# Optimization experiments

Hardware: AMD Instinct MI355X
Metric: run time of the kernel (lower is better)

## Reference

```python
import jax, jax.numpy as jnp
import numpy as np

TEMP = 0.07
W00 = 0.1
EPS = 1e-8


def setup_inputs() -> dict:
    key = jax.random.key(0)
    k1, k2, k3, k4 = jax.random.split(key, 4)
    B, N, D = 32, 256, 256
    M = B * N
    return {
        "audio_feats": jax.random.normal(k1, (B, N, D), dtype=jnp.float32),
        "visual_feats": jax.random.normal(k2, (B, N, D), dtype=jnp.float32),
        "audio_labels": jax.random.randint(k3, (M,), 0, 2, dtype=jnp.int64)
            if jax.config.jax_enable_x64 else jax.random.randint(k3, (M,), 0, 2, dtype=jnp.int32),
        "visual_labels": jax.random.randint(k4, (M,), 0, 2, dtype=jnp.int64)
            if jax.config.jax_enable_x64 else jax.random.randint(k4, (M,), 0, 2, dtype=jnp.int32),
    }


def reference(audio_feats, visual_feats, audio_labels, visual_labels):
    B, N, D = audio_feats.shape
    M = B * N
    a = audio_feats.reshape(M, D)
    v = visual_feats.reshape(M, D)
    # L2 normalize (torch F.normalize uses eps=1e-12 clamp on norm)
    a = a / jnp.maximum(jnp.linalg.norm(a, axis=-1, keepdims=True), 1e-12)
    v = v / jnp.maximum(jnp.linalg.norm(v, axis=-1, keepdims=True), 1e-12)
    sim = (a @ v.T) / TEMP  # (M, M)
    exp_sim = jnp.exp(sim)
    la = audio_labels[:, None]  # (M, 1)
    lv = visual_labels[None, :]  # (1, M)
    pos_mask = (la == lv) & ((la == 1) | (la == 0))
    weight = jnp.where(la == 1, 1.0, W00) * pos_mask.astype(sim.dtype)  # (M, M)
    wexp = exp_sim * weight

    # audio -> visual (row direction)
    denom_a2v = exp_sim.sum(axis=1)
    num_a2v = wexp.sum(axis=1)
    frac_a2v = (num_a2v + EPS) / (denom_a2v + EPS)
    valid_a2v = (num_a2v > 0).astype(sim.dtype)
    loss_a2v = -(valid_a2v * jnp.log(frac_a2v)).sum() / jnp.maximum(valid_a2v.sum(), 1.0)

    # visual -> audio (column direction)
    denom_v2a = exp_sim.sum(axis=0)
    num_v2a = wexp.sum(axis=0)
    frac_v2a = (num_v2a + EPS) / (denom_v2a + EPS)
    valid_v2a = (num_v2a > 0).astype(sim.dtype)
    loss_v2a = -(valid_v2a * jnp.log(frac_v2a)).sum() / jnp.maximum(valid_v2a.sum(), 1.0)

    return 0.5 * (loss_a2v + loss_v2a)
```

## Files before the change

kernel.cpp:

```cpp
#include <hip/hip_runtime.h>

#define M_ROWS 8192
#define D_DIM  256
#define BM     128
#define BN     128
#define NBI    (M_ROWS / BM)
#define NBJ    (M_ROWS / BN)
#define NJOBS  (NBI * NBJ)

#define ALPHA  4.53982478f


typedef __attribute__((ext_vector_type(4))) float floatx4;
typedef __attribute__((ext_vector_type(8))) int   intx8;

__device__ inline float fast_exp2(float x) {
#if __has_builtin(__builtin_amdgcn_exp2f)
    return __builtin_amdgcn_exp2f(x);
#else
    return exp2f(x);
#endif
}

__device__ inline floatx4 mfma_fp8(intx8 a, intx8 b, floatx4 c) {
    return __builtin_amdgcn_mfma_scale_f32_16x16x128_f8f6f4(
        a, b, c, 0, 0, 0, 0x7f7f7f7f, 0, 0x7f7f7f7f);
}

__global__ __launch_bounds__(256) void normalize_kernel(
    const float* __restrict__ af, const float* __restrict__ vf,
    unsigned char* __restrict__ aB, unsigned char* __restrict__ vB,
    float* __restrict__ glob)
{
    __shared__ float ssb[16][4];

    if (blockIdx.x == 0) {
        if (threadIdx.x < 4) glob[threadIdx.x] = 0.f;
        if (threadIdx.x == 4) ((int*)glob)[4] = 0;
    }

    const int b = blockIdx.x;
    const bool isA = b < 512;
    const int T = isA ? b : b - 512;
    const float* src = (isA ? af : vf) + (size_t)T * 16 * D_DIM;
    unsigned char* dst = (isA ? aB : vB) + (size_t)T * 4096;

    const int t    = threadIdx.x;
    const int wave = t >> 6, lane = t & 63;
    const int row  = t & 15;
    const int kq   = (t >> 4) & 3;
    const int h    = (t >> 6) & 1;
    const int s    = t >> 7;
    const int kbase = s * 128 + kq * 32 + h * 16;

    const float* p = src + row * D_DIM + kbase;
    float4 x0 = ((const float4*)p)[0], x1 = ((const float4*)p)[1];
    float4 x2 = ((const float4*)p)[2], x3 = ((const float4*)p)[3];

    float ss = x0.x*x0.x + x0.y*x0.y + x0.z*x0.z + x0.w*x0.w
             + x1.x*x1.x + x1.y*x1.y + x1.z*x1.z + x1.w*x1.w
             + x2.x*x2.x + x2.y*x2.y + x2.z*x2.z + x2.w*x2.w
             + x3.x*x3.x + x3.y*x3.y + x3.z*x3.z + x3.w*x3.w;
    ss += __shfl_xor(ss, 16, 64);
    ss += __shfl_xor(ss, 32, 64);
    if (lane < 16) ssb[lane][wave] = ss;
    __syncthreads();
    float tot = ssb[row][0] + ssb[row][1] + ssb[row][2] + ssb[row][3];
    float scale = ALPHA / fmaxf(sqrtf(tot), 1e-12f);

    int4 o;
    int pk;
    pk  = __builtin_amdgcn_cvt_pk_fp8_f32(x0.x*scale, x0.y*scale, 0, false);
    pk  = __builtin_amdgcn_cvt_pk_fp8_f32(x0.z*scale, x0.w*scale, pk, true);
    o.x = pk;
    pk  = __builtin_amdgcn_cvt_pk_fp8_f32(x1.x*scale, x1.y*scale, 0, false);
    pk  = __builtin_amdgcn_cvt_pk_fp8_f32(x1.z*scale, x1.w*scale, pk, true);
    o.y = pk;
    pk  = __builtin_amdgcn_cvt_pk_fp8_f32(x2.x*scale, x2.y*scale, 0, false);
    pk  = __builtin_amdgcn_cvt_pk_fp8_f32(x2.z*scale, x2.w*scale, pk, true);
    o.z = pk;
    pk  = __builtin_amdgcn_cvt_pk_fp8_f32(x3.x*scale, x3.y*scale, 0, false);
    pk  = __builtin_amdgcn_cvt_pk_fp8_f32(x3.z*scale, x3.w*scale, pk, true);
    o.w = pk;
    *(int4*)(dst + (size_t)t * 16) = o;
}

__global__ __launch_bounds__(256, 3) void gemm_loss_kernel(
    const unsigned char* __restrict__ aB, const unsigned char* __restrict__ vB,
    const int* __restrict__ la, const int* __restrict__ lv,
    float* __restrict__ rowPart, float* __restrict__ colPart)
{
    __shared__ unsigned char ldsB[32768];
    __shared__ float rowbuf[2 * BM];
    __shared__ float colbuf[8 * BN];

    const int tid  = threadIdx.x;
    const int wave = tid >> 6, lane = tid & 63;
    const int quad = lane >> 4, l16 = lane & 15;

    const int super = blockIdx.x >> 8;
    const int inner = blockIdx.x & 255;
    const int bx = (super & 3) * 16 + (inner & 15);
    const int by = (super >> 2) * 16 + (inner >> 4);
    const int i0 = bx * BM, j0 = by * BN;

    {
        const unsigned char* vsrc = vB + (size_t)by * 32768 + (size_t)wave * 8192
                                       + (size_t)lane * 16;
        unsigned char* ldst = ldsB + wave * 8192 + lane * 16;
        #pragma unroll
        for (int c = 0; c < 8; ++c)
            *(int4*)(ldst + c * 1024) = *(const int4*)(vsrc + c * 1024);
    }

    const unsigned char* Abase = aB + (size_t)(bx * 8 + wave * 2) * 4096
                                    + (size_t)lane * 16;
    intx8 afr[2][2];
    #pragma unroll
    for (int it = 0; it < 2; ++it) {
        #pragma unroll
        for (int s = 0; s < 2; ++s) {
            int4 h0 = *(const int4*)(Abase + it * 4096 + s * 2048);
            int4 h1 = *(const int4*)(Abase + it * 4096 + s * 2048 + 1024);
            afr[it][s] = intx8{h0.x, h0.y, h0.z, h0.w, h1.x, h1.y, h1.z, h1.w};
        }
    }

    __syncthreads();

    floatx4 acc[2][8] = {};
    const unsigned char* Bl = ldsB + lane * 16;
    #pragma unroll
    for (int s = 0; s < 2; ++s) {
        #pragma unroll
        for (int jt = 0; jt < 8; ++jt) {
            int4 h0 = *(const int4*)(Bl + jt * 4096 + s * 2048);
            int4 h1 = *(const int4*)(Bl + jt * 4096 + s * 2048 + 1024);
            intx8 bf = intx8{h0.x, h0.y, h0.z, h0.w, h1.x, h1.y, h1.z, h1.w};
            acc[0][jt] = mfma_fp8(afr[0][s], bf, acc[0][jt]);
            acc[1][jt] = mfma_fp8(afr[1][s], bf, acc[1][jt]);
        }
    }

    const int baseRow = i0 + wave * 32;
    float maf[2][4];
    #pragma unroll
    for (int it = 0; it < 2; ++it)
        #pragma unroll
        for (int r = 0; r < 4; ++r)
            maf[it][r] = (float)la[baseRow + it * 16 + quad * 4 + r];
    float mvf[8];
    #pragma unroll
    for (int jt = 0; jt < 8; ++jt)
        mvf[jt] = (float)lv[j0 + jt * 16 + l16];

    float rT[2][4] = {}, r1[2][4] = {};
    float cT[8] = {}, c1[8] = {};
    #pragma unroll
    for (int it = 0; it < 2; ++it) {
        #pragma unroll
        for (int jt = 0; jt < 8; ++jt) {
            #pragma unroll
            for (int r = 0; r < 4; ++r) {
                float e = fast_exp2(acc[it][jt][r]);
                rT[it][r] += e;
                r1[it][r] = fmaf(mvf[jt], e, r1[it][r]);
                cT[jt] += e;
                c1[jt] = fmaf(maf[it][r], e, c1[jt]);
            }
        }
    }

    #pragma unroll
    for (int jt = 0; jt < 8; ++jt) {
        float t0 = cT[jt], t1 = c1[jt];
        t0 += __shfl_xor(t0, 16, 64); t0 += __shfl_xor(t0, 32, 64);
        t1 += __shfl_xor(t1, 16, 64); t1 += __shfl_xor(t1, 32, 64);
        cT[jt] = t0; c1[jt] = t1;
    }

    #pragma unroll
    for (int it = 0; it < 2; ++it) {
        #pragma unroll
        for (int r = 0; r < 4; ++r) {
            float s0 = rT[it][r], s1 = r1[it][r];
            #pragma unroll
            for (int m = 1; m < 16; m <<= 1) {
                s0 += __shfl_xor(s0, m, 64);
                s1 += __shfl_xor(s1, m, 64);
            }
            if (l16 == 0) {
                int rl = wave * 32 + it * 16 + quad * 4 + r;
                rowbuf[rl * 2 + 0] = s0;
                rowbuf[rl * 2 + 1] = s1;
            }
        }
    }
    if (quad == 0) {
        #pragma unroll
        for (int jt = 0; jt < 8; ++jt) {
            colbuf[(wave * 2 + 0) * BN + jt * 16 + l16] = cT[jt];
            colbuf[(wave * 2 + 1) * BN + jt * 16 + l16] = c1[jt];
        }
    }
    __syncthreads();

    {
        const int rl  = tid >> 1;
        const int cls = tid & 1;
        rowPart[((size_t)by * M_ROWS + i0 + rl) * 2 + cls] = rowbuf[rl * 2 + cls];
        float s = colbuf[(0 * 2 + cls) * BN + rl] + colbuf[(1 * 2 + cls) * BN + rl]
                + colbuf[(2 * 2 + cls) * BN + rl] + colbuf[(3 * 2 + cls) * BN + rl];
        colPart[((size_t)bx * M_ROWS + j0 + rl) * 2 + cls] = s;
    }
}

__global__ __launch_bounds__(256) void reduce_kernel(
    const float* __restrict__ rowPart, const float* __restrict__ colPart,
    const int* __restrict__ la, const int* __restrict__ lv,
    float* __restrict__ glob, float* __restrict__ out)
{
    const int bid = blockIdx.x;
    const bool aside = bid < 32;
    const int idx = (aside ? bid : bid - 32) * 256 + threadIdx.x;
    const float* part = aside ? rowPart : colPart;
    const int* lab = aside ? la : lv;

    float tot = 0.f, c1 = 0.f;
    #pragma unroll 4
    for (int b = 0; b < 64; ++b) {
        float2 p = *(const float2*)(part + ((size_t)b * M_ROWS + idx) * 2);
        tot += p.x; c1 += p.y;
    }
    float num = lab[idx] ? c1 : 0.1f * (tot - c1);
    float lg = 0.f, cnt = 0.f;
    if (num > 0.f) { lg = logf((num + 1e-8f) / (tot + 1e-8f)); cnt = 1.f; }

    #pragma unroll
    for (int m = 1; m < 64; m <<= 1) {
        lg  += __shfl_xor(lg,  m, 64);
        cnt += __shfl_xor(cnt, m, 64);
    }
    __shared__ float red[4][2];
    const int w = threadIdx.x >> 6, ln = threadIdx.x & 63;
    if (ln == 0) { red[w][0] = lg; red[w][1] = cnt; }
    __syncthreads();
    if (threadIdx.x == 0) {
        float slg  = red[0][0] + red[1][0] + red[2][0] + red[3][0];
        float scnt = red[0][1] + red[1][1] + red[2][1] + red[3][1];
        float* base = glob + (aside ? 0 : 2);
        atomicAdd(&base[0], slg);
        atomicAdd(&base[1], scnt);
        __threadfence();
        int old = atomicAdd((int*)glob + 4, 1);
        if (old == 63) {
            __threadfence();
            float sA = atomicAdd(&glob[0], 0.f);
            float cA = atomicAdd(&glob[1], 0.f);
            float sV = atomicAdd(&glob[2], 0.f);
            float cV = atomicAdd(&glob[3], 0.f);
            float lossA = -sA / fmaxf(cA, 1.f);
            float lossV = -sV / fmaxf(cV, 1.f);
            out[0] = 0.5f * (lossA + lossV);
        }
    }
}

extern "C" void kernel_launch(void* const* d_in, const int* in_sizes, int n_in,
                              void* d_out, int out_size, void* d_ws, size_t ws_size,
                              hipStream_t stream)
{
    const float* af = (const float*)d_in[0];
    const float* vf = (const float*)d_in[1];
    const int*   la = (const int*)d_in[2];
    const int*   lv = (const int*)d_in[3];
    float* out = (float*)d_out;

    char* ws = (char*)d_ws;
    unsigned char* aB = (unsigned char*)ws;
    unsigned char* vB = (unsigned char*)(ws + 2ull * 1024 * 1024);
    float* rowPart   = (float*)(ws +  4ull * 1024 * 1024);
    float* colPart   = (float*)(ws +  8ull * 1024 * 1024);
    float* glob      = (float*)(ws + 12ull * 1024 * 1024);

    normalize_kernel<<<1024, 256, 0, stream>>>(af, vf, aB, vB, glob);
    gemm_loss_kernel<<<NJOBS, 256, 0, stream>>>(aB, vB, la, lv, rowPart, colPart);
    reduce_kernel<<<64, 256, 0, stream>>>(rowPart, colPart, la, lv, glob, out);
}
```

Before: 117.8 us.

## Widen column span per block with double-buffered async global-to-LDS B loads

Each block now covers 256 columns in four 64-column sub-tiles instead of one 128x128 tile. The B sub-tiles are streamed into a double-buffered LDS area with global_load_lds, so the next load overlaps the MFMA and exp work on the current one. This halves the block count and the rowPart slabs, and cuts the number of A-fragment reloads. In exchange it adds a barrier per sub-tile, drops the supertile swizzle used for L2 locality, and lowers parallelism, which may affect occupancy and load balance.

Result: slower. 174.3 us (+47.9%).

```diff
diff --git a/kernel.cpp b/kernel.cpp
--- a/kernel.cpp
+++ b/kernel.cpp
@@ -3,16 +3,21 @@
 #define M_ROWS 8192
 #define D_DIM  256
 #define BM     128
-#define BN     128
+#define JSPAN  256
 #define NBI    (M_ROWS / BM)
-#define NBJ    (M_ROWS / BN)
-#define NJOBS  (NBI * NBJ)
+#define NJQ    (M_ROWS / JSPAN)
+#define NJOBS  (NBI * NJQ)
 
 #define ALPHA  4.53982478f
 
 
 typedef __attribute__((ext_vector_type(4))) float floatx4;
 typedef __attribute__((ext_vector_type(8))) int   intx8;
+
+#define GLOAD_LDS16(gp, lp) \
+    __builtin_amdgcn_global_load_lds( \
+        (__attribute__((address_space(1))) void*)(gp), \
+        (__attribute__((address_space(3))) void*)(lp), 16, 0, 0)
 
 __device__ inline float fast_exp2(float x) {
 #if __has_builtin(__builtin_amdgcn_exp2f)
@@ -90,27 +95,24 @@
     const int* __restrict__ la, const int* __restrict__ lv,
     float* __restrict__ rowPart, float* __restrict__ colPart)
 {
-    __shared__ unsigned char ldsB[32768];
+    __shared__ unsigned char ldsB[2][16384];
     __shared__ float rowbuf[2 * BM];
-    __shared__ float colbuf[8 * BN];
+    __shared__ float colbuf[8 * JSPAN];
 
     const int tid  = threadIdx.x;
     const int wave = tid >> 6, lane = tid & 63;
     const int quad = lane >> 4, l16 = lane & 15;
 
-    const int super = blockIdx.x >> 8;
-    const int inner = blockIdx.x & 255;
-    const int bx = (super & 3) * 16 + (inner & 15);
-    const int by = (super >> 2) * 16 + (inner >> 4);
-    const int i0 = bx * BM, j0 = by * BN;
+    const int bx = blockIdx.x & 63;
+    const int jq = blockIdx.x >> 6;
+    const int i0 = bx * BM, j0 = jq * JSPAN;
 
     {
-        const unsigned char* vsrc = vB + (size_t)by * 32768 + (size_t)wave * 8192
-                                       + (size_t)lane * 16;
-        unsigned char* ldst = ldsB + wave * 8192 + lane * 16;
-        #pragma unroll
-        for (int c = 0; c < 8; ++c)
-            *(int4*)(ldst + c * 1024) = *(const int4*)(vsrc + c * 1024);
+        const unsigned char* src = vB + (size_t)jq * 65536 + (size_t)tid * 16;
+        unsigned char* dstl = &ldsB[0][0] + tid * 16;
+        #pragma unroll
+        for (int c = 0; c < 4; ++c)
+            GLOAD_LDS16(src + c * 4096, dstl + c * 4096);
     }
 
     const unsigned char* Abase = aB + (size_t)(bx * 8 + wave * 2) * 4096
@@ -126,22 +128,6 @@
         }
     }
 
-    __syncthreads();
-
-    floatx4 acc[2][8] = {};
-    const unsigned char* Bl = ldsB + lane * 16;
-    #pragma unroll
-    for (int s = 0; s < 2; ++s) {
-        #pragma unroll
-        for (int jt = 0; jt < 8; ++jt) {
-            int4 h0 = *(const int4*)(Bl + jt * 4096 + s * 2048);
-            int4 h1 = *(const int4*)(Bl + jt * 4096 + s * 2048 + 1024);
-            intx8 bf = intx8{h0.x, h0.y, h0.z, h0.w, h1.x, h1.y, h1.z, h1.w};
-            acc[0][jt] = mfma_fp8(afr[0][s], bf, acc[0][jt]);
-            acc[1][jt] = mfma_fp8(afr[1][s], bf, acc[1][jt]);
-        }
-    }
-
     const int baseRow = i0 + wave * 32;
     float maf[2][4];
     #pragma unroll
@@ -149,34 +135,66 @@
         #pragma unroll
         for (int r = 0; r < 4; ++r)
             maf[it][r] = (float)la[baseRow + it * 16 + quad * 4 + r];
-    float mvf[8];
-    #pragma unroll
-    for (int jt = 0; jt < 8; ++jt)
-        mvf[jt] = (float)lv[j0 + jt * 16 + l16];
+    float mvf[4][4];
+    #pragma unroll
+    for (int t = 0; t < 4; ++t)
+        #pragma unroll
+        for (int jt = 0; jt < 4; ++jt)
+            mvf[t][jt] = (float)lv[j0 + t * 64 + jt * 16 + l16];
 
     float rT[2][4] = {}, r1[2][4] = {};
-    float cT[8] = {}, c1[8] = {};
-    #pragma unroll
-    for (int it = 0; it < 2; ++it) {
-        #pragma unroll
-        for (int jt = 0; jt < 8; ++jt) {
+
+    #pragma unroll
+    for (int t = 0; t < 4; ++t) {
+        __syncthreads();
+        if (t < 3) {
+            const unsigned char* src = vB + (size_t)jq * 65536
+                                          + (size_t)(t + 1) * 16384 + (size_t)tid * 16;
+            unsigned char* dstl = &ldsB[(t + 1) & 1][0] + tid * 16;
             #pragma unroll
-            for (int r = 0; r < 4; ++r) {
-                float e = fast_exp2(acc[it][jt][r]);
-                rT[it][r] += e;
-                r1[it][r] = fmaf(mvf[jt], e, r1[it][r]);
-                cT[jt] += e;
-                c1[jt] = fmaf(maf[it][r], e, c1[jt]);
-            }
-        }
-    }
-
-    #pragma unroll
-    for (int jt = 0; jt < 8; ++jt) {
-        float t0 = cT[jt], t1 = c1[jt];
-        t0 += __shfl_xor(t0, 16, 64); t0 += __shfl_xor(t0, 32, 64);
-        t1 += __shfl_xor(t1, 16, 64); t1 += __shfl_xor(t1, 32, 64);
-        cT[jt] = t0; c1[jt] = t1;
+            for (int c = 0; c < 4; ++c)
+                GLOAD_LDS16(src + c * 4096, dstl + c * 4096);
+        }
+
+        floatx4 acc[2][4] = {};
+        const unsigned char* Bl = &ldsB[t & 1][0] + lane * 16;
+        #pragma unroll
+        for (int s = 0; s < 2; ++s) {
+            #pragma unroll
+            for (int jt = 0; jt < 4; ++jt) {
+                int4 h0 = *(const int4*)(Bl + jt * 4096 + s * 2048);
+                int4 h1 = *(const int4*)(Bl + jt * 4096 + s * 2048 + 1024);
+                intx8 bf = intx8{h0.x, h0.y, h0.z, h0.w, h1.x, h1.y, h1.z, h1.w};
+                acc[0][jt] = mfma_fp8(afr[0][s], bf, acc[0][jt]);
+                acc[1][jt] = mfma_fp8(afr[1][s], bf, acc[1][jt]);
+            }
+        }
+
+        float cT[4] = {}, c1[4] = {};
+        #pragma unroll
+        for (int it = 0; it < 2; ++it) {
+            #pragma unroll
+            for (int jt = 0; jt < 4; ++jt) {
+                #pragma unroll
+                for (int r = 0; r < 4; ++r) {
+                    float e = fast_exp2(acc[it][jt][r]);
+                    rT[it][r] += e;
+                    r1[it][r] = fmaf(mvf[t][jt], e, r1[it][r]);
+                    cT[jt] += e;
+                    c1[jt] = fmaf(maf[it][r], e, c1[jt]);
+                }
+            }
+        }
+        #pragma unroll
+        for (int jt = 0; jt < 4; ++jt) {
+            float t0 = cT[jt], t1 = c1[jt];
+            t0 += __shfl_xor(t0, 16, 64); t0 += __shfl_xor(t0, 32, 64);
+            t1 += __shfl_xor(t1, 16, 64); t1 += __shfl_xor(t1, 32, 64);
+            if (quad == 0) {
+                colbuf[(wave * 2 + 0) * JSPAN + t * 64 + jt * 16 + l16] = t0;
+                colbuf[(wave * 2 + 1) * JSPAN + t * 64 + jt * 16 + l16] = t1;
+            }
+        }
     }
 
     #pragma unroll
@@ -196,22 +214,21 @@
             }
         }
     }
-    if (quad == 0) {
-        #pragma unroll
-        for (int jt = 0; jt < 8; ++jt) {
-            colbuf[(wave * 2 + 0) * BN + jt * 16 + l16] = cT[jt];
-            colbuf[(wave * 2 + 1) * BN + jt * 16 + l16] = c1[jt];
-        }
-    }
     __syncthreads();
 
     {
         const int rl  = tid >> 1;
         const int cls = tid & 1;
-        rowPart[((size_t)by * M_ROWS + i0 + rl) * 2 + cls] = rowbuf[rl * 2 + cls];
-        float s = colbuf[(0 * 2 + cls) * BN + rl] + colbuf[(1 * 2 + cls) * BN + rl]
-                + colbuf[(2 * 2 + cls) * BN + rl] + colbuf[(3 * 2 + cls) * BN + rl];
-        colPart[((size_t)bx * M_ROWS + j0 + rl) * 2 + cls] = s;
+        rowPart[((size_t)jq * M_ROWS + i0 + rl) * 2 + cls] = rowbuf[rl * 2 + cls];
+
+        float sT = 0.f, s1 = 0.f;
+        #pragma unroll
+        for (int w = 0; w < 4; ++w) {
+            sT += colbuf[(w * 2 + 0) * JSPAN + tid];
+            s1 += colbuf[(w * 2 + 1) * JSPAN + tid];
+        }
+        float2 cv; cv.x = sT; cv.y = s1;
+        *(float2*)&colPart[((size_t)bx * M_ROWS + j0 + tid) * 2] = cv;
     }
 }
 
@@ -225,10 +242,11 @@
     const int idx = (aside ? bid : bid - 32) * 256 + threadIdx.x;
     const float* part = aside ? rowPart : colPart;
     const int* lab = aside ? la : lv;
+    const int nslab = aside ? NJQ : NBI;
 
     float tot = 0.f, c1 = 0.f;
     #pragma unroll 4
-    for (int b = 0; b < 64; ++b) {
+    for (int b = 0; b < nslab; ++b) {
         float2 p = *(const float2*)(part + ((size_t)b * M_ROWS + idx) * 2);
         tot += p.x; c1 += p.y;
     }
```
